# Performance work log

Measured on AMD Instinct MI355X. Metric: run time of the kernel, lower is better.

## Reference

```python
import jax, jax.numpy as jnp
import numpy as np

B = 64        # graphs per batch
N = 1024      # nodes per graph
DEG = 16      # avg degree
E = B * N * DEG
F_IN = 10
H = 128
NC = 10
K1, K2, K3 = 205, 41, 9   # ceil(0.2 * prev_nodes_per_graph)


def _lin(key, fan_in, shape):
    return jax.random.normal(key, shape, jnp.float32) * (1.0 / np.sqrt(fan_in))


def setup_inputs() -> dict:
    key = jax.random.key(0)
    ks = jax.random.split(key, 32)
    x = jax.random.normal(ks[0], (B * N, F_IN), jnp.float32)
    # random intra-graph edges (source_to_target)
    src_l = jax.random.randint(ks[1], (B, N * DEG), 0, N)
    dst_l = jax.random.randint(ks[2], (B, N * DEG), 0, N)
    off = (jnp.arange(B) * N)[:, None]
    edge_index = jnp.stack([(src_l + off).reshape(-1), (dst_l + off).reshape(-1)]).astype(jnp.int32)
    inp = dict(x=x, edge_index=edge_index)
    inp["W1"] = _lin(ks[3], F_IN, (F_IN, H)); inp["b1"] = jnp.zeros((H,), jnp.float32)
    inp["W2"] = _lin(ks[4], H, (H, H));       inp["b2"] = jnp.zeros((H,), jnp.float32)
    inp["W3"] = _lin(ks[5], H, (H, H));       inp["b3"] = jnp.zeros((H,), jnp.float32)
    inp["Ws1"] = _lin(ks[6], H, (H, 1)); inp["bs1"] = jnp.zeros((1,), jnp.float32)
    inp["Ws2"] = _lin(ks[7], H, (H, 1)); inp["bs2"] = jnp.zeros((1,), jnp.float32)
    inp["Ws3"] = _lin(ks[8], H, (H, 1)); inp["bs3"] = jnp.zeros((1,), jnp.float32)
    inp["Wl1"] = _lin(ks[9], 2 * H, (2 * H, H));    inp["bl1"] = jnp.zeros((H,), jnp.float32)
    inp["Wl2"] = _lin(ks[10], H, (H, H // 2));      inp["bl2"] = jnp.zeros((H // 2,), jnp.float32)
    inp["Wl3"] = _lin(ks[11], H // 2, (H // 2, NC)); inp["bl3"] = jnp.zeros((NC,), jnp.float32)
    return inp


def gcn(x, W, b, src, dst, emask, n):
    """PyG GCNConv: symmetric norm with self-loops; masked edges contribute 0."""
    h = x @ W                                   # [n, out]
    w = emask.astype(h.dtype)                   # edge weights (0 for filtered edges)
    deg = jax.ops.segment_sum(w, dst, num_segments=n) + 1.0   # +1 self-loop
    dis = jax.lax.rsqrt(deg)                    # deg^{-1/2}
    norm = dis[src] * dis[dst] * w              # [E]
    out = jax.ops.segment_sum(h[src] * norm[:, None], dst, num_segments=n)
    out = out + h * (dis * dis)[:, None]        # self-loop message
    return out + b


def sagpool(x, src, dst, emask, Ws, bs, cur, k):
    """SAGPool: GCN score -> per-graph top-k -> gather + tanh gate -> filter_adj."""
    n = B * cur
    score = gcn(x, Ws, bs, src, dst, emask, n)[:, 0]          # [n]
    _, idx = jax.lax.top_k(score.reshape(B, cur), k)          # [B, k]
    perm = (idx + (jnp.arange(B) * cur)[:, None]).reshape(-1) # global node ids
    x = x[perm] * jnp.tanh(score[perm])[:, None]
    # filter_adj: remap node ids, drop edges with an unselected endpoint
    new_id = jnp.full((n,), -1, jnp.int32).at[perm].set(jnp.arange(B * k, dtype=jnp.int32))
    nsrc, ndst = new_id[src], new_id[dst]
    emask = emask & (nsrc >= 0) & (ndst >= 0)
    nsrc = jnp.where(emask, nsrc, 0)
    ndst = jnp.where(emask, ndst, 0)
    return x, nsrc, ndst, emask


def readout(x, k):
    xb = x.reshape(B, k, -1)
    return jnp.concatenate([xb.max(axis=1), xb.mean(axis=1)], axis=1)   # [B, 2H]


def reference(x, edge_index, W1, b1, W2, b2, W3, b3,
              Ws1, bs1, Ws2, bs2, Ws3, bs3,
              Wl1, bl1, Wl2, bl2, Wl3, bl3):
    src, dst = edge_index[0], edge_index[1]
    emask = jnp.ones((E,), bool)

    h = jax.nn.relu(gcn(x, W1, b1, src, dst, emask, B * N))
    h, src, dst, emask = sagpool(h, src, dst, emask, Ws1, bs1, N, K1)
    x1 = readout(h, K1)

    h = jax.nn.relu(gcn(h, W2, b2, src, dst, emask, B * K1))
    h, src, dst, emask = sagpool(h, src, dst, emask, Ws2, bs2, K1, K2)
    x2 = readout(h, K2)

    h = jax.nn.relu(gcn(h, W3, b3, src, dst, emask, B * K2))
    h, src, dst, emask = sagpool(h, src, dst, emask, Ws3, bs3, K2, K3)
    x3 = readout(h, K3)

    z = x1 + x2 + x3                             # [B, 2H]
    z = jax.nn.relu(z @ Wl1 + bl1)               # dropout is eval-mode identity
    z = jax.nn.relu(z @ Wl2 + bl2)
    return jax.nn.log_softmax(z @ Wl3 + bl3, axis=-1)
```

## Files before the change

### kernel.cpp

```cpp
#include <hip/hip_runtime.h>
#include <math.h>

#define NB 64
#define N0 1024
#define NEDGE 1048576
#define EPG 16384
#define FIN 10
#define NCLS 10
#define KP1 205
#define KP2 41
#define KP3 9

static inline int ceil_div(int a, int b) { return (a + b - 1) / b; }

__global__ __launch_bounds__(1024) void build_csr1_k(const int* __restrict__ ei,
                                                     float* __restrict__ disg,
                                                     int* __restrict__ offg,
                                                     int* __restrict__ cntg,
                                                     int2* __restrict__ csr2) {
    __shared__ int cnt[N0];
    __shared__ int cur[N0];
    __shared__ float disl[N0];
    __shared__ int scan[1024];
    int b = blockIdx.x, t = threadIdx.x;
    cnt[t] = 0;
    __syncthreads();
    const int ebase = b * EPG;
    const int nbase = b * N0;
    #pragma unroll
    for (int u = 0; u < EPG / 1024; ++u) {
        int d = ei[NEDGE + ebase + u * 1024 + t] - nbase;
        atomicAdd(&cnt[d], 1);
    }
    __syncthreads();
    int v = cnt[t];
    scan[t] = v;
    __syncthreads();
    #pragma unroll
    for (int s = 1; s < 1024; s <<= 1) {
        int tv = (t >= s) ? scan[t - s] : 0;
        __syncthreads();
        scan[t] += tv;
        __syncthreads();
    }
    int excl = scan[t] - v;
    cur[t] = excl;
    float di = rsqrtf((float)v + 1.0f);
    disl[t] = di;
    offg[nbase + t] = ebase + excl;
    cntg[nbase + t] = v;
    disg[nbase + t] = di;
    __syncthreads();
    #pragma unroll
    for (int u = 0; u < EPG / 1024; ++u) {
        int j = ebase + u * 1024 + t;
        int s = ei[j], d = ei[NEDGE + j] - nbase;
        int pos = atomicAdd(&cur[d], 1);
        int2 o; o.x = s; o.y = __float_as_int(disl[s - nbase]);
        csr2[ebase + pos] = o;
    }
}

template <int CUR, int PREVK, bool COMPOSE>
__global__ __launch_bounds__(1024) void build_csrN_k(const int* __restrict__ ei,
                                                     const int* __restrict__ nid1,
                                                     const int* __restrict__ nid2,
                                                     float* __restrict__ disg,
                                                     int* __restrict__ offg,
                                                     int* __restrict__ cntg,
                                                     int2* __restrict__ csr2) {
    __shared__ int n1[N0];
    __shared__ int n2c[COMPOSE ? PREVK : 1];
    __shared__ int cnt[CUR];
    __shared__ int cur[CUR];
    __shared__ float disl[CUR];
    __shared__ int scan[1024];
    int b = blockIdx.x, t = threadIdx.x;
    n1[t] = nid1[b * N0 + t];
    if (COMPOSE && t < PREVK) n2c[t] = nid2[b * PREVK + t];
    if (t < CUR) cnt[t] = 0;
    __syncthreads();
    const int ebase = b * EPG;
    const int nbase = b * N0;
    auto mapn = [&](int l) -> int {
        int g1 = n1[l];
        if (g1 < 0) return -1;
        if (!COMPOSE) return g1 - b * CUR;
        int g2 = n2c[g1 - b * PREVK];
        return (g2 < 0) ? -1 : (g2 - b * CUR);
    };
    #pragma unroll
    for (int u = 0; u < EPG / 1024; ++u) {
        int j = ebase + u * 1024 + t;
        int s = ei[j] - nbase, d = ei[NEDGE + j] - nbase;
        int ld = mapn(d);
        if (ld < 0) continue;
        if (mapn(s) < 0) continue;
        atomicAdd(&cnt[ld], 1);
    }
    __syncthreads();
    int v = (t < CUR) ? cnt[t] : 0;
    scan[t] = v;
    __syncthreads();
    #pragma unroll
    for (int s = 1; s < 1024; s <<= 1) {
        int tv = (t >= s) ? scan[t - s] : 0;
        __syncthreads();
        scan[t] += tv;
        __syncthreads();
    }
    if (t < CUR) {
        int excl = scan[t] - v;
        cur[t] = excl;
        float di = rsqrtf((float)v + 1.0f);
        disl[t] = di;
        offg[b * CUR + t] = ebase + excl;
        cntg[b * CUR + t] = v;
        disg[b * CUR + t] = di;
    }
    __syncthreads();
    #pragma unroll
    for (int u = 0; u < EPG / 1024; ++u) {
        int j = ebase + u * 1024 + t;
        int s = ei[j] - nbase, d = ei[NEDGE + j] - nbase;
        int ld = mapn(d);
        if (ld < 0) continue;
        int ls = mapn(s);
        if (ls < 0) continue;
        int pos = atomicAdd(&cur[ld], 1);
        int2 o; o.x = b * CUR + ls; o.y = __float_as_int(disl[ls]);
        csr2[ebase + pos] = o;
    }
}

__global__ __launch_bounds__(256) void agg10_k(const float* __restrict__ x,
                                               const int2* __restrict__ csr2,
                                               const int* __restrict__ off,
                                               const int* __restrict__ cnt,
                                               const float* __restrict__ dis,
                                               float* __restrict__ y) {
    __shared__ float xl[N0 * 11];
    int b = blockIdx.x >> 2, chunk = blockIdx.x & 3;
    const float* xg = x + (size_t)b * (N0 * FIN);
    for (int u = threadIdx.x; u < N0 * FIN; u += 256) {
        int r = u / FIN, c = u - r * FIN;
        xl[r * 11 + c] = xg[u];
    }
    __syncthreads();
    int li = chunk * 256 + threadIdx.x;
    int i  = b * N0 + li;
    int s0 = off[i], m = cnt[i];
    int base = b * N0;
    float acc[FIN];
    #pragma unroll
    for (int f = 0; f < FIN; ++f) acc[f] = 0.f;
    int j = 0;
    for (; j + 2 <= m; j += 2) {
        int2 e0 = csr2[s0 + j], e1 = csr2[s0 + j + 1];
        int sl0 = (e0.x - base) * 11, sl1 = (e1.x - base) * 11;
        float w0 = __int_as_float(e0.y), w1 = __int_as_float(e1.y);
        #pragma unroll
        for (int f = 0; f < FIN; ++f) acc[f] += xl[sl0 + f] * w0 + xl[sl1 + f] * w1;
    }
    if (j < m) {
        int2 e0 = csr2[s0 + j];
        int sl0 = (e0.x - base) * 11;
        float w0 = __int_as_float(e0.y);
        #pragma unroll
        for (int f = 0; f < FIN; ++f) acc[f] += xl[sl0 + f] * w0;
    }
    float di = dis[i], d2 = di * di;
    #pragma unroll
    for (int f = 0; f < FIN; ++f)
        y[(size_t)i * FIN + f] = di * acc[f] + d2 * xl[li * 11 + f];
}

__global__ void gemm_fin_fused_k(const float* __restrict__ y, const float* __restrict__ W,
                                 const float* __restrict__ bb, const float* __restrict__ Wsc,
                                 const float* __restrict__ dis,
                                 float* __restrict__ hout, float* __restrict__ hs,
                                 float* __restrict__ hsd, int n) {
    __shared__ float Ws[FIN * 128];
    __shared__ float Sc[128];
    for (int u = threadIdx.x; u < FIN * 128; u += 256) Ws[u] = W[u];
    if (threadIdx.x < 128) Sc[threadIdx.x] = Wsc[threadIdx.x];
    __syncthreads();
    int t = blockIdx.x * 256 + threadIdx.x;
    int i = t >> 6, lane = threadIdx.x & 63;
    if (i >= n) return;
    float a = (lane < FIN) ? y[(size_t)i * FIN + lane] : 0.f;
    const float2* W2 = (const float2*)Ws;
    float ax = bb[lane * 2], ay = bb[lane * 2 + 1];
    #pragma unroll
    for (int k = 0; k < FIN; ++k) {
        float ak = __shfl(a, k);
        float2 w = W2[k * 64 + lane];
        ax += ak * w.x; ay += ak * w.y;
    }
    ax = fmaxf(ax, 0.f); ay = fmaxf(ay, 0.f);
    float2 o; o.x = ax; o.y = ay;
    ((float2*)hout)[(size_t)i * 64 + lane] = o;
    float part = ax * Sc[lane * 2] + ay * Sc[lane * 2 + 1];
    #pragma unroll
    for (int sh = 32; sh >= 1; sh >>= 1) part += __shfl_xor(part, sh);
    if (lane == 0) { hs[i] = part; hsd[i] = part * dis[i]; }
}

__global__ __launch_bounds__(256) void gemm128_tiled_k(const float* __restrict__ A,
                                                       const float* __restrict__ W,
                                                       float* __restrict__ C, int n) {
    __shared__ float As[64][33];
    __shared__ float Wt[32][64];
    int tx = threadIdx.x & 15, ty = threadIdx.x >> 4;
    int r0 = blockIdx.x * 64;
    int c0 = blockIdx.y * 64;
    float4 acc0 = {0,0,0,0}, acc1 = {0,0,0,0}, acc2 = {0,0,0,0}, acc3 = {0,0,0,0};
    int u = threadIdx.x;
    for (int k0 = 0; k0 < 128; k0 += 32) {
        __syncthreads();
        {
            int rr = u >> 3, cc = (u & 7) * 4;
            #pragma unroll
            for (int h = 0; h < 2; ++h) {
                int r = rr + h * 32;
                float4 v = {0,0,0,0};
                if (r0 + r < n) v = *(const float4*)&A[(size_t)(r0 + r) * 128 + k0 + cc];
                As[r][cc] = v.x; As[r][cc+1] = v.y; As[r][cc+2] = v.z; As[r][cc+3] = v.w;
            }
        }
        {
            int kk = u >> 4, c = (u & 15) * 4;
            #pragma unroll
            for (int h = 0; h < 2; ++h) {
                float4 v = *(const float4*)&W[(size_t)(k0 + kk + h * 16) * 128 + c0 + c];
                *(float4*)&Wt[kk + h * 16][c] = v;
            }
        }
        __syncthreads();
        #pragma unroll
        for (int kk = 0; kk < 32; ++kk) {
            float4 wv = *(const float4*)&Wt[kk][tx * 4];
            float a0 = As[ty * 4 + 0][kk];
            float a1 = As[ty * 4 + 1][kk];
            float a2 = As[ty * 4 + 2][kk];
            float a3 = As[ty * 4 + 3][kk];
            acc0.x += a0 * wv.x; acc0.y += a0 * wv.y; acc0.z += a0 * wv.z; acc0.w += a0 * wv.w;
            acc1.x += a1 * wv.x; acc1.y += a1 * wv.y; acc1.z += a1 * wv.z; acc1.w += a1 * wv.w;
            acc2.x += a2 * wv.x; acc2.y += a2 * wv.y; acc2.z += a2 * wv.z; acc2.w += a2 * wv.w;
            acc3.x += a3 * wv.x; acc3.y += a3 * wv.y; acc3.z += a3 * wv.z; acc3.w += a3 * wv.w;
        }
    }
    int r = r0 + ty * 4;
    if (r + 0 < n) *(float4*)&C[(size_t)(r + 0) * 128 + c0 + tx * 4] = acc0;
    if (r + 1 < n) *(float4*)&C[(size_t)(r + 1) * 128 + c0 + tx * 4] = acc1;
    if (r + 2 < n) *(float4*)&C[(size_t)(r + 2) * 128 + c0 + tx * 4] = acc2;
    if (r + 3 < n) *(float4*)&C[(size_t)(r + 3) * 128 + c0 + tx * 4] = acc3;
}

__global__ void gcn_agg_fused2_k(const float* __restrict__ hW, const int2* __restrict__ csr2,
                                 const int* __restrict__ off, const int* __restrict__ cnt,
                                 const float* __restrict__ dis, const float* __restrict__ bias,
                                 const float* __restrict__ Wsc,
                                 float* __restrict__ hout, float* __restrict__ hs,
                                 float* __restrict__ hsd, int n, int cpx) {
    int wg = ((blockIdx.x & 7) * cpx) + (blockIdx.x >> 3);
    int t = wg * blockDim.x + threadIdx.x;
    int i = t >> 6;
    int lane = threadIdx.x & 63;
    if (i >= n) return;
    const float2* hW2 = (const float2*)hW;
    int s0 = off[i], e0 = s0 + cnt[i];
    float accx = 0.f, accy = 0.f;
    for (int j0 = s0; j0 < e0; j0 += 64) {
        int rem = e0 - j0;
        int m = rem < 64 ? rem : 64;
        int sv = 0; float wv = 0.f;
        if (lane < m) { int2 ec = csr2[j0 + lane]; sv = ec.x; wv = __int_as_float(ec.y); }
        int u = 0;
        for (; u + 4 <= m; u += 4) {
            int a0 = __shfl(sv, u + 0), a1 = __shfl(sv, u + 1);
            int a2 = __shfl(sv, u + 2), a3 = __shfl(sv, u + 3);
            float w0 = __shfl(wv, u + 0), w1 = __shfl(wv, u + 1);
            float w2 = __shfl(wv, u + 2), w3 = __shfl(wv, u + 3);
            float2 v0 = hW2[(size_t)a0 * 64 + lane];
            float2 v1 = hW2[(size_t)a1 * 64 + lane];
            float2 v2 = hW2[(size_t)a2 * 64 + lane];
            float2 v3 = hW2[(size_t)a3 * 64 + lane];
            accx += v0.x * w0 + v1.x * w1 + v2.x * w2 + v3.x * w3;
            accy += v0.y * w0 + v1.y * w1 + v2.y * w2 + v3.y * w3;
        }
        for (; u < m; ++u) {
            int s = __shfl(sv, u);
            float w = __shfl(wv, u);
            float2 v = hW2[(size_t)s * 64 + lane];
            accx += v.x * w; accy += v.y * w;
        }
    }
    float di = dis[i];
    float2 hv = hW2[(size_t)i * 64 + lane];
    float ox = fmaxf(di * accx + hv.x * (di * di) + bias[lane * 2], 0.f);
    float oy = fmaxf(di * accy + hv.y * (di * di) + bias[lane * 2 + 1], 0.f);
    float2 o; o.x = ox; o.y = oy;
    ((float2*)hout)[(size_t)i * 64 + lane] = o;
    float part = ox * Wsc[lane * 2] + oy * Wsc[lane * 2 + 1];
    #pragma unroll
    for (int sh = 32; sh >= 1; sh >>= 1) part += __shfl_xor(part, sh);
    if (lane == 0) { hs[i] = part; hsd[i] = part * di; }
}

template <int CAP, int K>
__global__ void score_topk_pool_k(const float* __restrict__ hout,
                                  const float* __restrict__ hs, const float* __restrict__ hsd,
                                  const int2* __restrict__ csr2, const int* __restrict__ off,
                                  const int* __restrict__ cnt, const float* __restrict__ dis,
                                  const float* __restrict__ bs,
                                  float* __restrict__ hA, float* __restrict__ z,
                                  int* __restrict__ newid, int cur) {
    __shared__ float v[CAP];
    __shared__ int ix[CAP];
    __shared__ float zm[CAP];
    __shared__ float zs[CAP];
    __shared__ float hl[CAP];
    int b = blockIdx.x, t = threadIdx.x;
    if (t < cur) hl[t] = hsd[b * cur + t];
    __syncthreads();
    float sc = -INFINITY;
    if (t < cur) {
        int i = b * cur + t;
        int s0 = off[i], e0 = s0 + cnt[i];
        float acc = 0.f;
        int j = s0;
        for (; j + 4 <= e0; j += 4) {
            int x0 = csr2[j].x, x1 = csr2[j+1].x, x2 = csr2[j+2].x, x3 = csr2[j+3].x;
            acc += hl[x0 - b*cur] + hl[x1 - b*cur] + hl[x2 - b*cur] + hl[x3 - b*cur];
        }
        for (; j < e0; ++j) acc += hl[csr2[j].x - b*cur];
        float di = dis[i];
        sc = di * acc + hs[i] * (di * di) + bs[0];
    }
    v[t] = sc; ix[t] = t;
    __syncthreads();
    for (int size = 2; size <= CAP; size <<= 1) {
        for (int stride = size >> 1; stride > 0; stride >>= 1) {
            if (t < CAP / 2) {
                int pos = 2 * t - (t & (stride - 1));
                int j2 = pos + stride;
                bool asc = (pos & size) == 0;
                float v0 = v[pos], v1 = v[j2];
                int i0 = ix[pos], i1 = ix[j2];
                bool jb = (v1 > v0) || (v1 == v0 && i1 < i0);
                bool sw = asc ? jb : !jb;
                if (sw) { v[pos] = v1; v[j2] = v0; ix[pos] = i1; ix[j2] = i0; }
            }
            __syncthreads();
        }
    }
    if (t < K)            newid[b * cur + ix[t]] = b * K + t;
    else if (ix[t] < cur) newid[b * cur + ix[t]] = -1;
    if (t < K) zm[t] = tanhf(v[t]);
    __syncthreads();
    if constexpr (CAP >= 128) {
        const int G = CAP / 128;
        int g = t >> 7, f = t & 127;
        float vmax = -INFINITY, vsum = 0.f;
        for (int j = g; j < K; j += G) {
            int src = b * cur + ix[j];
            float val = hout[(size_t)src * 128 + f] * zm[j];
            hA[((size_t)b * K + j) * 128 + f] = val;
            vmax = fmaxf(vmax, val); vsum += val;
        }
        __syncthreads();
        zm[t] = vmax; zs[t] = vsum;
        __syncthreads();
        if (t < 128) {
            float m = zm[t], s2 = zs[t];
            for (int g2 = 1; g2 < G; ++g2) { m = fmaxf(m, zm[g2 * 128 + t]); s2 += zs[g2 * 128 + t]; }
            z[b * 256 + t] += m;
            z[b * 256 + 128 + t] += s2 / (float)K;
        }
    } else {
        float vmax0 = -INFINITY, vsum0 = 0.f, vmax1 = -INFINITY, vsum1 = 0.f;
        for (int j = 0; j < K; ++j) {
            int src = b * cur + ix[j];
            float gt = zm[j];
            float a = hout[(size_t)src * 128 + t] * gt;
            float c = hout[(size_t)src * 128 + 64 + t] * gt;
            hA[((size_t)b * K + j) * 128 + t] = a;
            hA[((size_t)b * K + j) * 128 + 64 + t] = c;
            vmax0 = fmaxf(vmax0, a); vsum0 += a;
            vmax1 = fmaxf(vmax1, c); vsum1 += c;
        }
        z[b * 256 + t] += vmax0;
        z[b * 256 + 64 + t] += vmax1;
        z[b * 256 + 128 + t] += vsum0 / (float)K;
        z[b * 256 + 192 + t] += vsum1 / (float)K;
    }
}

__global__ void mlp_head_k(const float* __restrict__ z,
                           const float* __restrict__ Wl1, const float* __restrict__ bl1,
                           const float* __restrict__ Wl2, const float* __restrict__ bl2,
                           const float* __restrict__ Wl3, const float* __restrict__ bl3,
                           float* __restrict__ out) {
    __shared__ float zr[256], h1[128], h2[64], lg[NCLS], red[2];
    int b = blockIdx.x, t = threadIdx.x;
    zr[t] = z[b * 256 + t];
    zr[t + 128] = z[b * 256 + 128 + t];
    __syncthreads();
    float acc = bl1[t];
    #pragma unroll 8
    for (int i = 0; i < 256; ++i) acc += zr[i] * Wl1[i * 128 + t];
    h1[t] = fmaxf(acc, 0.f);
    __syncthreads();
    if (t < 64) {
        float a2 = bl2[t];
        #pragma unroll 8
        for (int i = 0; i < 128; ++i) a2 += h1[i] * Wl2[i * 64 + t];
        h2[t] = fmaxf(a2, 0.f);
    }
    __syncthreads();
    if (t < NCLS) {
        float a3 = bl3[t];
        #pragma unroll 8
        for (int i = 0; i < 64; ++i) a3 += h2[i] * Wl3[i * NCLS + t];
        lg[t] = a3;
    }
    __syncthreads();
    if (t == 0) {
        float m = lg[0];
        for (int i = 1; i < NCLS; ++i) m = fmaxf(m, lg[i]);
        float s = 0.f;
        for (int i = 0; i < NCLS; ++i) s += expf(lg[i] - m);
        red[0] = m; red[1] = logf(s);
    }
    __syncthreads();
    if (t < NCLS) out[b * NCLS + t] = lg[t] - red[0] - red[1];
}

extern "C" void kernel_launch(void* const* d_in, const int* in_sizes, int n_in,
                              void* d_out, int out_size, void* d_ws, size_t ws_size,
                              hipStream_t stream) {
    const float* x   = (const float*)d_in[0];
    const int*   ei  = (const int*)d_in[1];
    const float* W1  = (const float*)d_in[2];  const float* b1  = (const float*)d_in[3];
    const float* W2  = (const float*)d_in[4];  const float* b2  = (const float*)d_in[5];
    const float* W3  = (const float*)d_in[6];  const float* b3  = (const float*)d_in[7];
    const float* Ws1 = (const float*)d_in[8];  const float* bs1 = (const float*)d_in[9];
    const float* Ws2 = (const float*)d_in[10]; const float* bs2 = (const float*)d_in[11];
    const float* Ws3 = (const float*)d_in[12]; const float* bs3 = (const float*)d_in[13];
    const float* Wl1 = (const float*)d_in[14]; const float* bl1 = (const float*)d_in[15];
    const float* Wl2 = (const float*)d_in[16]; const float* bl2 = (const float*)d_in[17];
    const float* Wl3 = (const float*)d_in[18]; const float* bl3 = (const float*)d_in[19];
    float* out = (float*)d_out;

    const int NMAX = NB * N0;
    const int N1 = NB * KP1;
    const int N2 = NB * KP2;

    char* p = (char*)d_ws;
    float* z      = (float*)p; p += (size_t)NB * 256 * 4;
    float* hW     = (float*)p; p += (size_t)N1 * 128 * 4;
    float* hout   = (float*)p; p += (size_t)NMAX * 128 * 4;
    float* hA     = (float*)p; p += (size_t)N1 * 128 * 4;
    float* y      = (float*)p; p += (size_t)NMAX * FIN * 4;
    float* dis    = (float*)p; p += (size_t)NMAX * 4;
    float* hs     = (float*)p; p += (size_t)NMAX * 4;
    float* hsd    = (float*)p; p += (size_t)NMAX * 4;
    int* newid1   = (int*)p;   p += (size_t)NMAX * 4;
    int* newid2   = (int*)p;   p += (size_t)N1 * 4;
    int* off      = (int*)p;   p += (size_t)NMAX * 4;
    int* cnt      = (int*)p;   p += (size_t)NMAX * 4;
    int2* csr2    = (int2*)p;  p += (size_t)NEDGE * 8;

    hipMemsetAsync(z, 0, (size_t)NB * 256 * 4, stream);

    build_csr1_k<<<NB, 1024, 0, stream>>>(ei, dis, off, cnt, csr2);
    agg10_k<<<NB * 4, 256, 0, stream>>>(x, csr2, off, cnt, dis, y);
    gemm_fin_fused_k<<<NMAX / 4, 256, 0, stream>>>(y, W1, b1, Ws1, dis, hout, hs, hsd, NMAX);
    score_topk_pool_k<1024, KP1><<<NB, 1024, 0, stream>>>(
        hout, hs, hsd, csr2, off, cnt, dis, bs1, hA, z, newid1, N0);

    build_csrN_k<KP1, KP1, false><<<NB, 1024, 0, stream>>>(ei, newid1, nullptr, dis, off, cnt, csr2);
    {
        dim3 g(ceil_div(N1, 64), 2);
        gemm128_tiled_k<<<g, 256, 0, stream>>>(hA, W2, hW, N1);
    }
    gcn_agg_fused2_k<<<N1 / 4, 256, 0, stream>>>(
        hW, csr2, off, cnt, dis, b2, Ws2, hout, hs, hsd, N1, N1 / 32);
    score_topk_pool_k<256, KP2><<<NB, 256, 0, stream>>>(
        hout, hs, hsd, csr2, off, cnt, dis, bs2, hA, z, newid2, KP1);

    build_csrN_k<KP2, KP1, true><<<NB, 1024, 0, stream>>>(ei, newid1, newid2, dis, off, cnt, csr2);
    {
        dim3 g(ceil_div(N2, 64), 2);
        gemm128_tiled_k<<<g, 256, 0, stream>>>(hA, W3, hW, N2);
    }
    gcn_agg_fused2_k<<<N2 / 4, 256, 0, stream>>>(
        hW, csr2, off, cnt, dis, b3, Ws3, hout, hs, hsd, N2, N2 / 32);
    score_topk_pool_k<64, KP3><<<NB, 64, 0, stream>>>(
        hout, hs, hsd, csr2, off, cnt, dis, bs3, hA, z, newid1, KP2);

    mlp_head_k<<<NB, 128, 0, stream>>>(z, Wl1, bl1, Wl2, bl2, Wl3, bl3, out);
}
```

Before: 297.0 us.

## Fuse stage-1 CSR build, aggregation, GEMM, scoring and top-k pooling into one kernel

Replaces four stage-1 kernels (CSR build, 10-feature aggregation, input GEMM, score/top-k pool) and a memset with a single per-graph 1024-thread kernel. Edge indices are kept in registers, the aggregated features, scores and sort buffers live in shared memory, and the y/dis/off/cnt global round trips disappear. The trade-off is only 64 blocks of heavy shared-memory use (~110KB), which limits occupancy and parallelism across the GPU. The memset of z is dropped on the assumption that the fused kernel writes z fully, and stage 1 now stores graph-local source indices in csr2.

```diff
diff --git a/kernel.cpp b/kernel.cpp
--- a/kernel.cpp
+++ b/kernel.cpp
@@ -13,28 +13,50 @@
 
 static inline int ceil_div(int a, int b) { return (a + b - 1) / b; }
 
-__global__ __launch_bounds__(1024) void build_csr1_k(const int* __restrict__ ei,
-                                                     float* __restrict__ disg,
-                                                     int* __restrict__ offg,
-                                                     int* __restrict__ cntg,
-                                                     int2* __restrict__ csr2) {
-    __shared__ int cnt[N0];
-    __shared__ int cur[N0];
+__global__ __launch_bounds__(1024) void stage1_mega_k(
+    const float* __restrict__ x, const int* __restrict__ ei,
+    const float* __restrict__ W1, const float* __restrict__ b1,
+    const float* __restrict__ Ws1, const float* __restrict__ bs1,
+    float* __restrict__ hout, float* __restrict__ hA, float* __restrict__ z,
+    int* __restrict__ newid1, int2* __restrict__ csr2) {
+    __shared__ float xl[N0 * 11];
+    __shared__ float yl[N0 * 11];
+    __shared__ float Wl[FIN * 128];
+    __shared__ float Sc[128];
+    __shared__ int   cnt[N0];
     __shared__ float disl[N0];
-    __shared__ int scan[1024];
+    __shared__ int   scan[1024];
+    __shared__ float v[1024];
+    __shared__ int   ix[1024];
+    __shared__ float zm[1024];
+    __shared__ float zs[1024];
+    __shared__ float hsl[N0];
+    __shared__ float hsdl[N0];
+
     int b = blockIdx.x, t = threadIdx.x;
+    const int ebase = b * EPG, nbase = b * N0;
+
+    for (int u = t; u < FIN * 128; u += 1024) Wl[u] = W1[u];
+    if (t < 128) Sc[t] = Ws1[t];
+    const float* xg = x + (size_t)nbase * FIN;
+    for (int u = t; u < N0 * FIN; u += 1024) {
+        int r = u / FIN, c = u - r * FIN;
+        xl[r * 11 + c] = xg[u];
+    }
     cnt[t] = 0;
     __syncthreads();
-    const int ebase = b * EPG;
-    const int nbase = b * N0;
+
+    int sloc[EPG / 1024], dloc[EPG / 1024];
     #pragma unroll
     for (int u = 0; u < EPG / 1024; ++u) {
-        int d = ei[NEDGE + ebase + u * 1024 + t] - nbase;
-        atomicAdd(&cnt[d], 1);
-    }
-    __syncthreads();
-    int v = cnt[t];
-    scan[t] = v;
+        int j = ebase + u * 1024 + t;
+        sloc[u] = ei[j] - nbase;
+        dloc[u] = ei[NEDGE + j] - nbase;
+        atomicAdd(&cnt[dloc[u]], 1);
+    }
+    __syncthreads();
+    int deg = cnt[t];
+    scan[t] = deg;
     __syncthreads();
     #pragma unroll
     for (int s = 1; s < 1024; s <<= 1) {
@@ -43,21 +65,131 @@
         scan[t] += tv;
         __syncthreads();
     }
-    int excl = scan[t] - v;
-    cur[t] = excl;
-    float di = rsqrtf((float)v + 1.0f);
+    int strt = scan[t] - deg;
+    float di = rsqrtf((float)deg + 1.0f);
     disl[t] = di;
-    offg[nbase + t] = ebase + excl;
-    cntg[nbase + t] = v;
-    disg[nbase + t] = di;
-    __syncthreads();
+    __syncthreads();
+    cnt[t] = strt;
+    __syncthreads();
+
     #pragma unroll
     for (int u = 0; u < EPG / 1024; ++u) {
-        int j = ebase + u * 1024 + t;
-        int s = ei[j], d = ei[NEDGE + j] - nbase;
-        int pos = atomicAdd(&cur[d], 1);
-        int2 o; o.x = s; o.y = __float_as_int(disl[s - nbase]);
+        int pos = atomicAdd(&cnt[dloc[u]], 1);
+        int2 o; o.x = sloc[u]; o.y = __float_as_int(disl[sloc[u]]);
         csr2[ebase + pos] = o;
+    }
+    __syncthreads();
+
+    {
+        float acc[FIN];
+        #pragma unroll
+        for (int f = 0; f < FIN; ++f) acc[f] = 0.f;
+        const int2* cp = csr2 + ebase + strt;
+        int j = 0;
+        for (; j + 2 <= deg; j += 2) {
+            int2 e0 = cp[j], e1 = cp[j + 1];
+            int sl0 = e0.x * 11, sl1 = e1.x * 11;
+            float w0 = __int_as_float(e0.y), w1 = __int_as_float(e1.y);
+            #pragma unroll
+            for (int f = 0; f < FIN; ++f) acc[f] += xl[sl0 + f] * w0 + xl[sl1 + f] * w1;
+        }
+        if (j < deg) {
+            int2 e0 = cp[j];
+            int sl0 = e0.x * 11;
+            float w0 = __int_as_float(e0.y);
+            #pragma unroll
+            for (int f = 0; f < FIN; ++f) acc[f] += xl[sl0 + f] * w0;
+        }
+        float d2 = di * di;
+        #pragma unroll
+        for (int f = 0; f < FIN; ++f)
+            yl[t * 11 + f] = di * acc[f] + d2 * xl[t * 11 + f];
+    }
+    __syncthreads();
+
+    {
+        int f = t & 127, ng = t >> 7;
+        float bf = b1[f];
+        float* hp = hout + (size_t)nbase * 128;
+        #pragma unroll 4
+        for (int g = 0; g < 128; ++g) {
+            int n = g * 8 + ng;
+            float o = bf;
+            #pragma unroll
+            for (int k = 0; k < FIN; ++k) o += yl[n * 11 + k] * Wl[k * 128 + f];
+            hp[g * 1024 + t] = fmaxf(o, 0.f);
+        }
+    }
+    __syncthreads();
+
+    {
+        int w = t >> 6, lane = t & 63;
+        const float2* hp = (const float2*)(hout + (size_t)nbase * 128);
+        for (int it = 0; it < 64; ++it) {
+            int n = it * 16 + w;
+            float2 h2 = hp[n * 64 + lane];
+            float part = h2.x * Sc[lane * 2] + h2.y * Sc[lane * 2 + 1];
+            #pragma unroll
+            for (int sh = 32; sh >= 1; sh >>= 1) part += __shfl_xor(part, sh);
+            if (lane == 0) { hsl[n] = part; hsdl[n] = part * disl[n]; }
+        }
+    }
+    __syncthreads();
+
+    {
+        const int2* cp = csr2 + ebase + strt;
+        float acc = 0.f;
+        int j = 0;
+        for (; j + 4 <= deg; j += 4) {
+            int a0 = cp[j].x, a1 = cp[j+1].x, a2 = cp[j+2].x, a3 = cp[j+3].x;
+            acc += hsdl[a0] + hsdl[a1] + hsdl[a2] + hsdl[a3];
+        }
+        for (; j < deg; ++j) acc += hsdl[cp[j].x];
+        v[t] = di * acc + hsl[t] * (di * di) + bs1[0];
+        ix[t] = t;
+    }
+    __syncthreads();
+
+    for (int size = 2; size <= 1024; size <<= 1) {
+        for (int stride = size >> 1; stride > 0; stride >>= 1) {
+            if (t < 512) {
+                int pos = 2 * t - (t & (stride - 1));
+                int j2 = pos + stride;
+                bool asc = (pos & size) == 0;
+                float v0 = v[pos], v1 = v[j2];
+                int i0 = ix[pos], i1 = ix[j2];
+                bool jb = (v1 > v0) || (v1 == v0 && i1 < i0);
+                bool sw = asc ? jb : !jb;
+                if (sw) { v[pos] = v1; v[j2] = v0; ix[pos] = i1; ix[j2] = i0; }
+            }
+            __syncthreads();
+        }
+    }
+
+    if (t < KP1) newid1[nbase + ix[t]] = b * KP1 + t;
+    else         newid1[nbase + ix[t]] = -1;
+    if (t < KP1) zm[t] = tanhf(v[t]);
+    __syncthreads();
+
+    {
+        int g = t >> 7, f = t & 127;
+        float vmax = -INFINITY, vsum = 0.f;
+        for (int j = g; j < KP1; j += 8) {
+            int src = nbase + ix[j];
+            float val = hout[(size_t)src * 128 + f] * zm[j];
+            hA[((size_t)b * KP1 + j) * 128 + f] = val;
+            vmax = fmaxf(vmax, val); vsum += val;
+        }
+        __syncthreads();
+        zm[t] = vmax; zs[t] = vsum;
+        __syncthreads();
+        if (t < 128) {
+            float m = zm[t], s2 = zs[t];
+            #pragma unroll
+            for (int g2 = 1; g2 < 8; ++g2) { m = fmaxf(m, zm[g2 * 128 + t]); s2 += zs[g2 * 128 + t]; }
+            z[b * 256 + t] = m;
+            z[b * 256 + 128 + t] = s2 / (float)KP1;
+        }
     }
 }
 
@@ -131,79 +263,6 @@
         int2 o; o.x = b * CUR + ls; o.y = __float_as_int(disl[ls]);
         csr2[ebase + pos] = o;
     }
-}
-
-__global__ __launch_bounds__(256) void agg10_k(const float* __restrict__ x,
-                                               const int2* __restrict__ csr2,
-                                               const int* __restrict__ off,
-                                               const int* __restrict__ cnt,
-                                               const float* __restrict__ dis,
-                                               float* __restrict__ y) {
-    __shared__ float xl[N0 * 11];
-    int b = blockIdx.x >> 2, chunk = blockIdx.x & 3;
-    const float* xg = x + (size_t)b * (N0 * FIN);
-    for (int u = threadIdx.x; u < N0 * FIN; u += 256) {
-        int r = u / FIN, c = u - r * FIN;
-        xl[r * 11 + c] = xg[u];
-    }
-    __syncthreads();
-    int li = chunk * 256 + threadIdx.x;
-    int i  = b * N0 + li;
-    int s0 = off[i], m = cnt[i];
-    int base = b * N0;
-    float acc[FIN];
-    #pragma unroll
-    for (int f = 0; f < FIN; ++f) acc[f] = 0.f;
-    int j = 0;
-    for (; j + 2 <= m; j += 2) {
-        int2 e0 = csr2[s0 + j], e1 = csr2[s0 + j + 1];
-        int sl0 = (e0.x - base) * 11, sl1 = (e1.x - base) * 11;
-        float w0 = __int_as_float(e0.y), w1 = __int_as_float(e1.y);
-        #pragma unroll
-        for (int f = 0; f < FIN; ++f) acc[f] += xl[sl0 + f] * w0 + xl[sl1 + f] * w1;
-    }
-    if (j < m) {
-        int2 e0 = csr2[s0 + j];
-        int sl0 = (e0.x - base) * 11;
-        float w0 = __int_as_float(e0.y);
-        #pragma unroll
-        for (int f = 0; f < FIN; ++f) acc[f] += xl[sl0 + f] * w0;
-    }
-    float di = dis[i], d2 = di * di;
-    #pragma unroll
-    for (int f = 0; f < FIN; ++f)
-        y[(size_t)i * FIN + f] = di * acc[f] + d2 * xl[li * 11 + f];
-}
-
-__global__ void gemm_fin_fused_k(const float* __restrict__ y, const float* __restrict__ W,
-                                 const float* __restrict__ bb, const float* __restrict__ Wsc,
-                                 const float* __restrict__ dis,
-                                 float* __restrict__ hout, float* __restrict__ hs,
-                                 float* __restrict__ hsd, int n) {
-    __shared__ float Ws[FIN * 128];
-    __shared__ float Sc[128];
-    for (int u = threadIdx.x; u < FIN * 128; u += 256) Ws[u] = W[u];
-    if (threadIdx.x < 128) Sc[threadIdx.x] = Wsc[threadIdx.x];
-    __syncthreads();
-    int t = blockIdx.x * 256 + threadIdx.x;
-    int i = t >> 6, lane = threadIdx.x & 63;
-    if (i >= n) return;
-    float a = (lane < FIN) ? y[(size_t)i * FIN + lane] : 0.f;
-    const float2* W2 = (const float2*)Ws;
-    float ax = bb[lane * 2], ay = bb[lane * 2 + 1];
-    #pragma unroll
-    for (int k = 0; k < FIN; ++k) {
-        float ak = __shfl(a, k);
-        float2 w = W2[k * 64 + lane];
-        ax += ak * w.x; ay += ak * w.y;
-    }
-    ax = fmaxf(ax, 0.f); ay = fmaxf(ay, 0.f);
-    float2 o; o.x = ax; o.y = ay;
-    ((float2*)hout)[(size_t)i * 64 + lane] = o;
-    float part = ax * Sc[lane * 2] + ay * Sc[lane * 2 + 1];
-    #pragma unroll
-    for (int sh = 32; sh >= 1; sh >>= 1) part += __shfl_xor(part, sh);
-    if (lane == 0) { hs[i] = part; hsd[i] = part * dis[i]; }
 }
 
 __global__ __launch_bounds__(256) void gemm128_tiled_k(const float* __restrict__ A,
@@ -462,7 +521,6 @@
     float* hW     = (float*)p; p += (size_t)N1 * 128 * 4;
     float* hout   = (float*)p; p += (size_t)NMAX * 128 * 4;
     float* hA     = (float*)p; p += (size_t)N1 * 128 * 4;
-    float* y      = (float*)p; p += (size_t)NMAX * FIN * 4;
     float* dis    = (float*)p; p += (size_t)NMAX * 4;
     float* hs     = (float*)p; p += (size_t)NMAX * 4;
     float* hsd    = (float*)p; p += (size_t)NMAX * 4;
@@ -472,13 +530,8 @@
     int* cnt      = (int*)p;   p += (size_t)NMAX * 4;
     int2* csr2    = (int2*)p;  p += (size_t)NEDGE * 8;
 
-    hipMemsetAsync(z, 0, (size_t)NB * 256 * 4, stream);
-
-    build_csr1_k<<<NB, 1024, 0, stream>>>(ei, dis, off, cnt, csr2);
-    agg10_k<<<NB * 4, 256, 0, stream>>>(x, csr2, off, cnt, dis, y);
-    gemm_fin_fused_k<<<NMAX / 4, 256, 0, stream>>>(y, W1, b1, Ws1, dis, hout, hs, hsd, NMAX);
-    score_topk_pool_k<1024, KP1><<<NB, 1024, 0, stream>>>(
-        hout, hs, hsd, csr2, off, cnt, dis, bs1, hA, z, newid1, N0);
+    stage1_mega_k<<<NB, 1024, 0, stream>>>(x, ei, W1, b1, Ws1, bs1,
+                                           hout, hA, z, newid1, csr2);
 
     build_csrN_k<KP1, KP1, false><<<NB, 1024, 0, stream>>>(ei, newid1, nullptr, dis, off, cnt, csr2);
     {
```

Result: slower. 311.9 us (+5.0%).

## Fuse top-k pooling with next-level CSR build and final MLP head

Applied to the files above, without the earlier changes.

Merges each score/top-k/pool kernel with the following CSR-construction kernel, so the new node mapping is kept in shared memory and the edge list is filtered in the same block. This drops separate launches, the newid2 global round trip and the z memset, since stage one now writes z instead of accumulating into it. The last pooling stage is also fused into the MLP head. In exchange, every fused block runs at 1024 threads with large shared-memory footprints, including a 256-wide sort held inside a 1024-thread block, and the edge loop now runs serially after the sort within one block per graph.

```diff
diff --git a/kernel.cpp b/kernel.cpp
--- a/kernel.cpp
+++ b/kernel.cpp
@@ -57,78 +57,6 @@
         int s = ei[j], d = ei[NEDGE + j] - nbase;
         int pos = atomicAdd(&cur[d], 1);
         int2 o; o.x = s; o.y = __float_as_int(disl[s - nbase]);
-        csr2[ebase + pos] = o;
-    }
-}
-
-template <int CUR, int PREVK, bool COMPOSE>
-__global__ __launch_bounds__(1024) void build_csrN_k(const int* __restrict__ ei,
-                                                     const int* __restrict__ nid1,
-                                                     const int* __restrict__ nid2,
-                                                     float* __restrict__ disg,
-                                                     int* __restrict__ offg,
-                                                     int* __restrict__ cntg,
-                                                     int2* __restrict__ csr2) {
-    __shared__ int n1[N0];
-    __shared__ int n2c[COMPOSE ? PREVK : 1];
-    __shared__ int cnt[CUR];
-    __shared__ int cur[CUR];
-    __shared__ float disl[CUR];
-    __shared__ int scan[1024];
-    int b = blockIdx.x, t = threadIdx.x;
-    n1[t] = nid1[b * N0 + t];
-    if (COMPOSE && t < PREVK) n2c[t] = nid2[b * PREVK + t];
-    if (t < CUR) cnt[t] = 0;
-    __syncthreads();
-    const int ebase = b * EPG;
-    const int nbase = b * N0;
-    auto mapn = [&](int l) -> int {
-        int g1 = n1[l];
-        if (g1 < 0) return -1;
-        if (!COMPOSE) return g1 - b * CUR;
-        int g2 = n2c[g1 - b * PREVK];
-        return (g2 < 0) ? -1 : (g2 - b * CUR);
-    };
-    #pragma unroll
-    for (int u = 0; u < EPG / 1024; ++u) {
-        int j = ebase + u * 1024 + t;
-        int s = ei[j] - nbase, d = ei[NEDGE + j] - nbase;
-        int ld = mapn(d);
-        if (ld < 0) continue;
-        if (mapn(s) < 0) continue;
-        atomicAdd(&cnt[ld], 1);
-    }
-    __syncthreads();
-    int v = (t < CUR) ? cnt[t] : 0;
-    scan[t] = v;
-    __syncthreads();
-    #pragma unroll
-    for (int s = 1; s < 1024; s <<= 1) {
-        int tv = (t >= s) ? scan[t - s] : 0;
-        __syncthreads();
-        scan[t] += tv;
-        __syncthreads();
-    }
-    if (t < CUR) {
-        int excl = scan[t] - v;
-        cur[t] = excl;
-        float di = rsqrtf((float)v + 1.0f);
-        disl[t] = di;
-        offg[b * CUR + t] = ebase + excl;
-        cntg[b * CUR + t] = v;
-        disg[b * CUR + t] = di;
-    }
-    __syncthreads();
-    #pragma unroll
-    for (int u = 0; u < EPG / 1024; ++u) {
-        int j = ebase + u * 1024 + t;
-        int s = ei[j] - nbase, d = ei[NEDGE + j] - nbase;
-        int ld = mapn(d);
-        if (ld < 0) continue;
-        int ls = mapn(s);
-        if (ls < 0) continue;
-        int pos = atomicAdd(&cur[ld], 1);
-        int2 o; o.x = b * CUR + ls; o.y = __float_as_int(disl[ls]);
         csr2[ebase + pos] = o;
     }
 }
@@ -204,6 +132,129 @@
     #pragma unroll
     for (int sh = 32; sh >= 1; sh >>= 1) part += __shfl_xor(part, sh);
     if (lane == 0) { hs[i] = part; hsd[i] = part * dis[i]; }
+}
+
+__global__ __launch_bounds__(1024) void s1_topk_build2_k(
+    const float* __restrict__ hout, const float* __restrict__ hs,
+    const float* __restrict__ hsd, const int* __restrict__ ei,
+    int2* __restrict__ csr,
+    const int* __restrict__ off1, const int* __restrict__ cnt1,
+    const float* __restrict__ dis1, const float* __restrict__ bs1,
+    float* __restrict__ hA, float* __restrict__ z, int* __restrict__ newid1,
+    int* __restrict__ off2, int* __restrict__ cnt2g, float* __restrict__ dis2g) {
+    __shared__ float v[1024];
+    __shared__ int   ix[1024];
+    __shared__ float zm[1024];
+    __shared__ float zs[1024];
+    __shared__ float hl[1024];
+    __shared__ int   n1l[1024];
+    __shared__ int   c2[KP1];
+    __shared__ int   cur2[KP1];
+    __shared__ float d2l[KP1];
+    __shared__ int   scan[1024];
+    int b = blockIdx.x, t = threadIdx.x;
+    const int nbase = b * N0, ebase = b * EPG;
+
+    hl[t] = hsd[nbase + t];
+    __syncthreads();
+    {
+        int s0 = off1[nbase + t], e0 = s0 + cnt1[nbase + t];
+        float acc = 0.f;
+        int j = s0;
+        for (; j + 4 <= e0; j += 4) {
+            int a0 = csr[j].x, a1 = csr[j+1].x, a2 = csr[j+2].x, a3 = csr[j+3].x;
+            acc += hl[a0 - nbase] + hl[a1 - nbase] + hl[a2 - nbase] + hl[a3 - nbase];
+        }
+        for (; j < e0; ++j) acc += hl[csr[j].x - nbase];
+        float di = dis1[nbase + t];
+        v[t] = di * acc + hs[nbase + t] * (di * di) + bs1[0];
+        ix[t] = t;
+    }
+    __syncthreads();
+    for (int size = 2; size <= 1024; size <<= 1) {
+        for (int stride = size >> 1; stride > 0; stride >>= 1) {
+            if (t < 512) {
+                int pos = 2 * t - (t & (stride - 1));
+                int j2 = pos + stride;
+                bool asc = (pos & size) == 0;
+                float v0 = v[pos], v1 = v[j2];
+                int i0 = ix[pos], i1 = ix[j2];
+                bool jb = (v1 > v0) || (v1 == v0 && i1 < i0);
+                bool sw = asc ? jb : !jb;
+                if (sw) { v[pos] = v1; v[j2] = v0; ix[pos] = i1; ix[j2] = i0; }
+            }
+            __syncthreads();
+        }
+    }
+    {
+        int node = ix[t];
+        int loc = (t < KP1) ? t : -1;
+        n1l[node] = loc;
+        newid1[nbase + node] = (t < KP1) ? (b * KP1 + t) : -1;
+        if (t < KP1) zm[t] = tanhf(v[t]);
+    }
+    __syncthreads();
+    {
+        int g = t >> 7, f = t & 127;
+        float vmax = -INFINITY, vsum = 0.f;
+        for (int j = g; j < KP1; j += 8) {
+            int src = nbase + ix[j];
+            float val = hout[(size_t)src * 128 + f] * zm[j];
+            hA[((size_t)b * KP1 + j) * 128 + f] = val;
+            vmax = fmaxf(vmax, val); vsum += val;
+        }
+        __syncthreads();
+        zm[t] = vmax; zs[t] = vsum;
+        __syncthreads();
+        if (t < 128) {
+            float m = zm[t], s2 = zs[t];
+            #pragma unroll
+            for (int g2 = 1; g2 < 8; ++g2) { m = fmaxf(m, zm[g2 * 128 + t]); s2 += zs[g2 * 128 + t]; }
+            z[b * 256 + t] = m;
+            z[b * 256 + 128 + t] = s2 / (float)KP1;
+        }
+    }
+    __syncthreads();
+    if (t < KP1) c2[t] = 0;
+    __syncthreads();
+    int sl[EPG / 1024], dl[EPG / 1024];
+    #pragma unroll
+    for (int u = 0; u < EPG / 1024; ++u) {
+        int j = ebase + u * 1024 + t;
+        int s = ei[j] - nbase, d = ei[NEDGE + j] - nbase;
+        int ls = n1l[s], ld = n1l[d];
+        bool alive = (ls >= 0 && ld >= 0);
+        sl[u] = alive ? ls : -1; dl[u] = ld;
+        if (alive) atomicAdd(&c2[ld], 1);
+    }
+    __syncthreads();
+    int vv = (t < KP1) ? c2[t] : 0;
+    scan[t] = vv;
+    __syncthreads();
+    #pragma unroll
+    for (int s = 1; s < 1024; s <<= 1) {
+        int tv = (t >= s) ? scan[t - s] : 0;
+        __syncthreads();
+        scan[t] += tv;
+        __syncthreads();
+    }
+    if (t < KP1) {
+        int excl = scan[t] - vv;
+        cur2[t] = excl;
+        float dd = rsqrtf((float)vv + 1.0f);
+        d2l[t] = dd;
+        off2[b * KP1 + t] = ebase + excl;
+        cnt2g[b * KP1 + t] = vv;
+        dis2g[b * KP1 + t] = dd;
+    }
+    __syncthreads();
+    #pragma unroll
+    for (int u = 0; u < EPG / 1024; ++u) {
+        if (sl[u] < 0) continue;
+        int pos = atomicAdd(&cur2[dl[u]], 1);
+        int2 o; o.x = b * KP1 + sl[u]; o.y = __float_as_int(d2l[sl[u]]);
+        csr[ebase + pos] = o;
+    }
 }
 
 __global__ __launch_bounds__(256) void gemm128_tiled_k(const float* __restrict__ A,
@@ -308,41 +359,51 @@
     if (lane == 0) { hs[i] = part; hsd[i] = part * di; }
 }
 
-template <int CAP, int K>
-__global__ void score_topk_pool_k(const float* __restrict__ hout,
-                                  const float* __restrict__ hs, const float* __restrict__ hsd,
-                                  const int2* __restrict__ csr2, const int* __restrict__ off,
-                                  const int* __restrict__ cnt, const float* __restrict__ dis,
-                                  const float* __restrict__ bs,
-                                  float* __restrict__ hA, float* __restrict__ z,
-                                  int* __restrict__ newid, int cur) {
-    __shared__ float v[CAP];
-    __shared__ int ix[CAP];
-    __shared__ float zm[CAP];
-    __shared__ float zs[CAP];
-    __shared__ float hl[CAP];
+__global__ __launch_bounds__(1024) void s2_topk_build3_k(
+    const float* __restrict__ hout, const float* __restrict__ hs,
+    const float* __restrict__ hsd, const int* __restrict__ ei,
+    int2* __restrict__ csr,
+    const int* __restrict__ off2, const int* __restrict__ cnt2,
+    const float* __restrict__ dis2, const float* __restrict__ bs2,
+    const int* __restrict__ newid1,
+    float* __restrict__ hA, float* __restrict__ z,
+    int* __restrict__ off3, int* __restrict__ cnt3g, float* __restrict__ dis3g) {
+    __shared__ float v[256];
+    __shared__ int   ix[256];
+    __shared__ float hl[256];
+    __shared__ float zm[1024];
+    __shared__ float zs[1024];
+    __shared__ int   n1g[1024];
+    __shared__ int   n2l[KP1];
+    __shared__ int   c3[KP2];
+    __shared__ int   cur3[KP2];
+    __shared__ float d3l[KP2];
+    __shared__ int   scan[1024];
     int b = blockIdx.x, t = threadIdx.x;
-    if (t < cur) hl[t] = hsd[b * cur + t];
+    const int nbase = b * N0, ebase = b * EPG;
+
+    if (t < KP1) hl[t] = hsd[b * KP1 + t];
+    { int g1 = newid1[nbase + t]; n1g[t] = (g1 >= 0) ? (g1 - b * KP1) : -1; }
     __syncthreads();
     float sc = -INFINITY;
-    if (t < cur) {
-        int i = b * cur + t;
-        int s0 = off[i], e0 = s0 + cnt[i];
+    if (t < KP1) {
+        int i = b * KP1 + t;
+        int s0 = off2[i], e0 = s0 + cnt2[i];
         float acc = 0.f;
         int j = s0;
         for (; j + 4 <= e0; j += 4) {
-            int x0 = csr2[j].x, x1 = csr2[j+1].x, x2 = csr2[j+2].x, x3 = csr2[j+3].x;
-            acc += hl[x0 - b*cur] + hl[x1 - b*cur] + hl[x2 - b*cur] + hl[x3 - b*cur];
-        }
-        for (; j < e0; ++j) acc += hl[csr2[j].x - b*cur];
-        float di = dis[i];
-        sc = di * acc + hs[i] * (di * di) + bs[0];
-    }
-    v[t] = sc; ix[t] = t;
-    __syncthreads();
-    for (int size = 2; size <= CAP; size <<= 1) {
+            int a0 = csr[j].x, a1 = csr[j+1].x, a2 = csr[j+2].x, a3 = csr[j+3].x;
+            acc += hl[a0 - b*KP1] + hl[a1 - b*KP1] + hl[a2 - b*KP1] + hl[a3 - b*KP1];
+        }
+        for (; j < e0; ++j) acc += hl[csr[j].x - b*KP1];
+        float di = dis2[i];
+        sc = di * acc + hs[i] * (di * di) + bs2[0];
+    }
+    if (t < 256) { v[t] = sc; ix[t] = t; }
+    __syncthreads();
+    for (int size = 2; size <= 256; size <<= 1) {
         for (int stride = size >> 1; stride > 0; stride >>= 1) {
-            if (t < CAP / 2) {
+            if (t < 128) {
                 int pos = 2 * t - (t & (stride - 1));
                 int j2 = pos + stride;
                 bool asc = (pos & size) == 0;
@@ -355,18 +416,16 @@
             __syncthreads();
         }
     }
-    if (t < K)            newid[b * cur + ix[t]] = b * K + t;
-    else if (ix[t] < cur) newid[b * cur + ix[t]] = -1;
-    if (t < K) zm[t] = tanhf(v[t]);
-    __syncthreads();
-    if constexpr (CAP >= 128) {
-        const int G = CAP / 128;
+    if (t < 256) { int node = ix[t]; if (node < KP1) n2l[node] = (t < KP2) ? t : -1; }
+    if (t < KP2) zm[t] = tanhf(v[t]);
+    __syncthreads();
+    {
         int g = t >> 7, f = t & 127;
         float vmax = -INFINITY, vsum = 0.f;
-        for (int j = g; j < K; j += G) {
-            int src = b * cur + ix[j];
+        for (int j = g; j < KP2; j += 8) {
+            int src = b * KP1 + ix[j];
             float val = hout[(size_t)src * 128 + f] * zm[j];
-            hA[((size_t)b * K + j) * 128 + f] = val;
+            hA[((size_t)b * KP2 + j) * 128 + f] = val;
             vmax = fmaxf(vmax, val); vsum += val;
         }
         __syncthreads();
@@ -374,38 +433,115 @@
         __syncthreads();
         if (t < 128) {
             float m = zm[t], s2 = zs[t];
-            for (int g2 = 1; g2 < G; ++g2) { m = fmaxf(m, zm[g2 * 128 + t]); s2 += zs[g2 * 128 + t]; }
+            #pragma unroll
+            for (int g2 = 1; g2 < 8; ++g2) { m = fmaxf(m, zm[g2 * 128 + t]); s2 += zs[g2 * 128 + t]; }
             z[b * 256 + t] += m;
-            z[b * 256 + 128 + t] += s2 / (float)K;
-        }
-    } else {
-        float vmax0 = -INFINITY, vsum0 = 0.f, vmax1 = -INFINITY, vsum1 = 0.f;
-        for (int j = 0; j < K; ++j) {
-            int src = b * cur + ix[j];
-            float gt = zm[j];
-            float a = hout[(size_t)src * 128 + t] * gt;
-            float c = hout[(size_t)src * 128 + 64 + t] * gt;
-            hA[((size_t)b * K + j) * 128 + t] = a;
-            hA[((size_t)b * K + j) * 128 + 64 + t] = c;
-            vmax0 = fmaxf(vmax0, a); vsum0 += a;
-            vmax1 = fmaxf(vmax1, c); vsum1 += c;
-        }
-        z[b * 256 + t] += vmax0;
-        z[b * 256 + 64 + t] += vmax1;
-        z[b * 256 + 128 + t] += vsum0 / (float)K;
-        z[b * 256 + 192 + t] += vsum1 / (float)K;
-    }
-}
-
-__global__ void mlp_head_k(const float* __restrict__ z,
-                           const float* __restrict__ Wl1, const float* __restrict__ bl1,
-                           const float* __restrict__ Wl2, const float* __restrict__ bl2,
-                           const float* __restrict__ Wl3, const float* __restrict__ bl3,
-                           float* __restrict__ out) {
+            z[b * 256 + 128 + t] += s2 / (float)KP2;
+        }
+    }
+    __syncthreads();
+    if (t < KP2) c3[t] = 0;
+    __syncthreads();
+    int sl[EPG / 1024], dl[EPG / 1024];
+    #pragma unroll
+    for (int u = 0; u < EPG / 1024; ++u) {
+        int j = ebase + u * 1024 + t;
+        int s = ei[j] - nbase, d = ei[NEDGE + j] - nbase;
+        int a = n1g[s], bb = n1g[d];
+        int ls = -1, ld = -1;
+        if (a >= 0 && bb >= 0) { ls = n2l[a]; ld = n2l[bb]; }
+        bool alive = (ls >= 0 && ld >= 0);
+        sl[u] = alive ? ls : -1; dl[u] = ld;
+        if (alive) atomicAdd(&c3[ld], 1);
+    }
+    __syncthreads();
+    int vv = (t < KP2) ? c3[t] : 0;
+    scan[t] = vv;
+    __syncthreads();
+    #pragma unroll
+    for (int s = 1; s < 1024; s <<= 1) {
+        int tv = (t >= s) ? scan[t - s] : 0;
+        __syncthreads();
+        scan[t] += tv;
+        __syncthreads();
+    }
+    if (t < KP2) {
+        int excl = scan[t] - vv;
+        cur3[t] = excl;
+        float dd = rsqrtf((float)vv + 1.0f);
+        d3l[t] = dd;
+        off3[b * KP2 + t] = ebase + excl;
+        cnt3g[b * KP2 + t] = vv;
+        dis3g[b * KP2 + t] = dd;
+    }
+    __syncthreads();
+    #pragma unroll
+    for (int u = 0; u < EPG / 1024; ++u) {
+        if (sl[u] < 0) continue;
+        int pos = atomicAdd(&cur3[dl[u]], 1);
+        int2 o; o.x = b * KP2 + sl[u]; o.y = __float_as_int(d3l[sl[u]]);
+        csr[ebase + pos] = o;
+    }
+}
+
+__global__ __launch_bounds__(128) void s3_topk_mlp_k(
+    const float* __restrict__ hout, const float* __restrict__ hs,
+    const float* __restrict__ hsd, const int2* __restrict__ csr,
+    const int* __restrict__ off3, const int* __restrict__ cnt3,
+    const float* __restrict__ dis3, const float* __restrict__ bs3,
+    const float* __restrict__ z,
+    const float* __restrict__ Wl1, const float* __restrict__ bl1,
+    const float* __restrict__ Wl2, const float* __restrict__ bl2,
+    const float* __restrict__ Wl3, const float* __restrict__ bl3,
+    float* __restrict__ out) {
+    __shared__ float hl[KP2];
+    __shared__ float v[64];
+    __shared__ int   ix[64];
+    __shared__ float zm[KP3];
     __shared__ float zr[256], h1[128], h2[64], lg[NCLS], red[2];
     int b = blockIdx.x, t = threadIdx.x;
-    zr[t] = z[b * 256 + t];
-    zr[t + 128] = z[b * 256 + 128 + t];
+
+    if (t < KP2) hl[t] = hsd[b * KP2 + t];
+    __syncthreads();
+    float sc = -INFINITY;
+    if (t < KP2) {
+        int i = b * KP2 + t;
+        int s0 = off3[i], e0 = s0 + cnt3[i];
+        float acc = 0.f;
+        for (int j = s0; j < e0; ++j) acc += hl[csr[j].x - b*KP2];
+        float di = dis3[i];
+        sc = di * acc + hs[i] * (di * di) + bs3[0];
+    }
+    if (t < 64) { v[t] = sc; ix[t] = t; }
+    __syncthreads();
+    for (int size = 2; size <= 64; size <<= 1) {
+        for (int stride = size >> 1; stride > 0; stride >>= 1) {
+            if (t < 32) {
+                int pos = 2 * t - (t & (stride - 1));
+                int j2 = pos + stride;
+                bool asc = (pos & size) == 0;
+                float v0 = v[pos], v1 = v[j2];
+                int i0 = ix[pos], i1 = ix[j2];
+                bool jb = (v1 > v0) || (v1 == v0 && i1 < i0);
+                bool sw = asc ? jb : !jb;
+                if (sw) { v[pos] = v1; v[j2] = v0; ix[pos] = i1; ix[j2] = i0; }
+            }
+            __syncthreads();
+        }
+    }
+    if (t < KP3) zm[t] = tanhf(v[t]);
+    __syncthreads();
+    {
+        float vmax = -INFINITY, vsum = 0.f;
+        #pragma unroll
+        for (int j = 0; j < KP3; ++j) {
+            int src = b * KP2 + ix[j];
+            float val = hout[(size_t)src * 128 + t] * zm[j];
+            vmax = fmaxf(vmax, val); vsum += val;
+        }
+        zr[t] = z[b * 256 + t] + vmax;
+        zr[128 + t] = z[b * 256 + 128 + t] + vsum / (float)KP3;
+    }
     __syncthreads();
     float acc = bl1[t];
     #pragma unroll 8
@@ -463,42 +599,41 @@
     float* hout   = (float*)p; p += (size_t)NMAX * 128 * 4;
     float* hA     = (float*)p; p += (size_t)N1 * 128 * 4;
     float* y      = (float*)p; p += (size_t)NMAX * FIN * 4;
-    float* dis    = (float*)p; p += (size_t)NMAX * 4;
+    float* dis1   = (float*)p; p += (size_t)NMAX * 4;
     float* hs     = (float*)p; p += (size_t)NMAX * 4;
     float* hsd    = (float*)p; p += (size_t)NMAX * 4;
     int* newid1   = (int*)p;   p += (size_t)NMAX * 4;
-    int* newid2   = (int*)p;   p += (size_t)N1 * 4;
-    int* off      = (int*)p;   p += (size_t)NMAX * 4;
-    int* cnt      = (int*)p;   p += (size_t)NMAX * 4;
+    int* off1     = (int*)p;   p += (size_t)NMAX * 4;
+    int* cnt1     = (int*)p;   p += (size_t)NMAX * 4;
+    int* off2     = (int*)p;   p += (size_t)N1 * 4;
+    int* cnt2     = (int*)p;   p += (size_t)N1 * 4;
+    float* dis2   = (float*)p; p += (size_t)N1 * 4;
+    int* off3     = (int*)p;   p += (size_t)N2 * 4;
+    int* cnt3     = (int*)p;   p += (size_t)N2 * 4;
+    float* dis3   = (float*)p; p += (size_t)N2 * 4;
     int2* csr2    = (int2*)p;  p += (size_t)NEDGE * 8;
 
-    hipMemsetAsync(z, 0, (size_t)NB * 256 * 4, stream);
-
-    build_csr1_k<<<NB, 1024, 0, stream>>>(ei, dis, off, cnt, csr2);
-    agg10_k<<<NB * 4, 256, 0, stream>>>(x, csr2, off, cnt, dis, y);
-    gemm_fin_fused_k<<<NMAX / 4, 256, 0, stream>>>(y, W1, b1, Ws1, dis, hout, hs, hsd, NMAX);
-    score_topk_pool_k<1024, KP1><<<NB, 1024, 0, stream>>>(
-        hout, hs, hsd, csr2, off, cnt, dis, bs1, hA, z, newid1, N0);
-
-    build_csrN_k<KP1, KP1, false><<<NB, 1024, 0, stream>>>(ei, newid1, nullptr, dis, off, cnt, csr2);
+    build_csr1_k<<<NB, 1024, 0, stream>>>(ei, dis1, off1, cnt1, csr2);
+    agg10_k<<<NB * 4, 256, 0, stream>>>(x, csr2, off1, cnt1, dis1, y);
+    gemm_fin_fused_k<<<NMAX / 4, 256, 0, stream>>>(y, W1, b1, Ws1, dis1, hout, hs, hsd, NMAX);
+    s1_topk_build2_k<<<NB, 1024, 0, stream>>>(hout, hs, hsd, ei, csr2, off1, cnt1, dis1,
+                                              bs1, hA, z, newid1, off2, cnt2, dis2);
+
     {
         dim3 g(ceil_div(N1, 64), 2);
         gemm128_tiled_k<<<g, 256, 0, stream>>>(hA, W2, hW, N1);
     }
     gcn_agg_fused2_k<<<N1 / 4, 256, 0, stream>>>(
-        hW, csr2, off, cnt, dis, b2, Ws2, hout, hs, hsd, N1, N1 / 32);
-    score_topk_pool_k<256, KP2><<<NB, 256, 0, stream>>>(
-        hout, hs, hsd, csr2, off, cnt, dis, bs2, hA, z, newid2, KP1);
-
-    build_csrN_k<KP2, KP1, true><<<NB, 1024, 0, stream>>>(ei, newid1, newid2, dis, off, cnt, csr2);
+        hW, csr2, off2, cnt2, dis2, b2, Ws2, hout, hs, hsd, N1, N1 / 32);
+    s2_topk_build3_k<<<NB, 1024, 0, stream>>>(hout, hs, hsd, ei, csr2, off2, cnt2, dis2,
+                                              bs2, newid1, hA, z, off3, cnt3, dis3);
+
     {
         dim3 g(ceil_div(N2, 64), 2);
         gemm128_tiled_k<<<g, 256, 0, stream>>>(hA, W3, hW, N2);
     }
     gcn_agg_fused2_k<<<N2 / 4, 256, 0, stream>>>(
-        hW, csr2, off, cnt, dis, b3, Ws3, hout, hs, hsd, N2, N2 / 32);
-    score_topk_pool_k<64, KP3><<<NB, 64, 0, stream>>>(
-        hout, hs, hsd, csr2, off, cnt, dis, bs3, hA, z, newid1, KP2);
-
-    mlp_head_k<<<NB, 128, 0, stream>>>(z, Wl1, bl1, Wl2, bl2, Wl3, bl3, out);
-}
+        hW, csr2, off3, cnt3, dis3, b3, Ws3, hout, hs, hsd, N2, N2 / 32);
+    s3_topk_mlp_k<<<NB, 128, 0, stream>>>(hout, hs, hsd, csr2, off3, cnt3, dis3, bs3, z,
+                                          Wl1, bl1, Wl2, bl2, Wl3, bl3, out);
+}
```

Result: faster. 271.7 us (-8.5%).
